# Optimization experiments

Hardware: AMD Instinct MI355X
Metric: run time of the kernel (lower is better)

## Reference

```python
import jax, jax.numpy as jnp
import numpy as np
import math

SR = 96000.0
FRAME = 2048
NB = 16
GAIN_RANGE = (-24.0, 24.0)
Q_RANGE = (0.5, 16.0)
BROADBAND = (-60.0, 0.0)
HPF_R = (20.0, 500.0)
LPF_R = (5000.0, 20000.0)
SHELF_R = (50.0, 16000.0)
PEAK_R = (100.0, 15000.0)


def _dfreq(n, rng):
    lo, hi = math.log(rng[0]), math.log(rng[1])
    return jnp.exp(lo + n * (hi - lo))


def _dgain(n, rng=GAIN_RANGE):
    return rng[0] + n * (rng[1] - rng[0])


def _dq(n):
    lo, hi = math.log(Q_RANGE[0]), math.log(Q_RANGE[1])
    return jnp.exp(lo + n * (hi - lo))


def _coeffs(ftype, fc, gain_db, Q):
    # returns stacked [g, k, a1, a2, a3, m0, m1, m2], each same shape as fc
    g = jnp.clip(jnp.tan(math.pi * fc / SR), 1e-6, 100.0)
    Q = jnp.clip(Q, 0.1, 100.0)
    one = jnp.ones_like(g)
    zero = jnp.zeros_like(g)
    if ftype in ('highpass', 'lowpass'):
        k = 1.0 / Q
        a1 = 1.0 / (1.0 + g * (g + k)); a2 = g * a1; a3 = g * a2
        if ftype == 'highpass':
            m0, m1, m2 = one, -k, -one
        else:
            m0, m1, m2 = zero, zero, one
    elif ftype == 'peak':
        A = jnp.power(10.0, gain_db / 40.0)
        k = jnp.where(gain_db >= 0, 1.0 / (Q * A), A / Q)
        a1 = 1.0 / (1.0 + g * (g + k)); a2 = g * a1; a3 = g * a2
        m0, m1, m2 = one, k * (A * A - 1.0), zero
    elif ftype == 'lowshelf':
        A = jnp.power(10.0, gain_db / 40.0); sA = jnp.sqrt(A); k = 1.0 / Q
        gs = jnp.where(gain_db >= 0, g / sA, g * sA)
        a1 = 1.0 / (1.0 + gs * (gs + k)); a2 = gs * a1; a3 = gs * a2
        m0, m1, m2 = one, k * (A - 1.0), A * A - 1.0
    else:  # highshelf
        A = jnp.power(10.0, gain_db / 40.0); sA = jnp.sqrt(A); k = 1.0 / Q
        gs = jnp.where(gain_db >= 0, g * sA, g / sA)
        a1 = 1.0 / (1.0 + gs * (gs + k)); a2 = gs * a1; a3 = gs * a2
        m0, m1, m2 = A * A, k * (1.0 - A) * A, 1.0 - A * A
    return jnp.stack([g, k, a1, a2, a3, m0, m1, m2], 0)


def _all_coeffs(params, n_frames_audio):
    # params: (B, 50, n_frames_params) -> coeffs (nF, NB, 8, B), in/out gains (nF, B)
    B = params.shape[0]
    nFp = params.shape[2]
    pidx = jnp.minimum(jnp.arange(n_frames_audio), nFp - 1)
    fp = jnp.take(params, pidx, axis=2)                 # (B, 50, nF)
    bq = fp[:, :NB * 3, :].reshape(B, NB, 3, n_frames_audio)
    in_g = jnp.power(10.0, _dgain(fp[:, -2, :], BROADBAND) / 20.0)   # (B, nF)
    out_g = jnp.power(10.0, _dgain(fp[:, -1, :], BROADBAND) / 20.0)  # (B, nF)
    cs = []
    for i in range(NB):
        fn, gn, qn = bq[:, i, 0], bq[:, i, 1], bq[:, i, 2]  # (B, nF)
        Q = _dq(qn)
        if i == 0:
            c = _coeffs('highpass', _dfreq(fn, HPF_R), None, Q)
        elif i == 15:
            c = _coeffs('lowpass', _dfreq(fn, LPF_R), None, Q)
        elif i == 1:
            c = _coeffs('lowshelf', _dfreq(fn, SHELF_R), _dgain(gn), Q)
        elif i == 14:
            c = _coeffs('highshelf', _dfreq(fn, SHELF_R), _dgain(gn), Q)
        else:
            c = _coeffs('peak', _dfreq(fn, PEAK_R), _dgain(gn), Q)
        cs.append(c)  # (8, B, nF)
    coeffs = jnp.transpose(jnp.stack(cs, 0), (3, 0, 1, 2))  # (nF, NB, 8, B)
    return coeffs, in_g.T, out_g.T


def _forward(audio, params):
    B, S = audio.shape
    nF = S // FRAME  # S chosen as exact multiple of FRAME
    coeffs, in_g, out_g = _all_coeffs(params, nF)
    frames = jnp.transpose(audio.reshape(B, nF, FRAME), (1, 2, 0))  # (nF, FRAME, B)

    def frame_step(states, xs):
        fr, c, ig, og = xs  # fr (FRAME,B), c (NB,8,B), ig (B,), og (B,)
        x = fr * ig[None, :]
        new_states = []
        for i in range(NB):
            a1, a2, a3 = c[i, 2], c[i, 3], c[i, 4]
            m0, m1, m2 = c[i, 5], c[i, 6], c[i, 7]

            def samp(st, xn, a1=a1, a2=a2, a3=a3, m0=m0, m1=m1, m2=m2):
                ic1, ic2 = st
                v3 = xn - ic2
                v1 = a1 * ic1 + a2 * v3
                v2 = ic2 + a2 * v1 + a3 * v3
                out = m0 * xn + m1 * v1 + m2 * v2
                return (2.0 * v1 - ic1, 2.0 * v2 - ic2), out

            (ic1, ic2), x = jax.lax.scan(samp, (states[i, 0], states[i, 1]), x)
            new_states.append(jnp.stack([ic1, ic2], 0))
        return jnp.stack(new_states, 0), x * og[None, :]

    init = jnp.zeros((NB, 2, B), audio.dtype)
    _, out = jax.lax.scan(frame_step, init, (frames, coeffs, in_g, out_g))
    return jnp.transpose(out, (2, 0, 1)).reshape(B, S)  # (B, S)


_forward_jit = jax.jit(_forward)


def setup_inputs() -> dict:
    key = jax.random.key(0)
    k1, k2 = jax.random.split(key)
    B, S, nFp = 32, 49152, 24  # 24 frames of 2048 samples
    audio = jax.random.normal(k1, (B, S), dtype=jnp.float32) * 0.1
    params = jax.random.uniform(k2, (B, 50, nFp), dtype=jnp.float32)
    return {'audio': audio, 'params': params}


def reference(audio, params):
    return _forward_jit(audio, params)
```

## Files before the change

### kernel.cpp

```cpp
#include <hip/hip_runtime.h>
#include <math.h>

#define NBATCH 32
#define S      49152
#define NF     24
#define NB     16
#define CHUNK  32
#define NCH    768
#define NWAVE  12

__device__ __forceinline__ float clampf(float x, float lo, float hi) {
    return fminf(fmaxf(x, lo), hi);
}

#define FOREACH_S(OP) \
    OP(s00) OP(s01) OP(s02) OP(s03) OP(s04) OP(s05) OP(s06) OP(s07) \
    OP(s08) OP(s09) OP(s10) OP(s11) OP(s12) OP(s13) OP(s14) OP(s15) \
    OP(s16) OP(s17) OP(s18) OP(s19) OP(s20) OP(s21) OP(s22) OP(s23) \
    OP(s24) OP(s25) OP(s26) OP(s27) OP(s28) OP(s29) OP(s30) OP(s31)

#define DECL_S(x) float x;

#define STEPA(x) { \
    const float n1_ = fmaf(t00, ic1, fmaf(t01, ic2, b0 * (x))); \
    const float n2_ = fmaf(t10, ic1, fmaf(t11, ic2, b1 * (x))); \
    ic1 = n1_; ic2 = n2_; }

#define STEPC(x) { \
    const float y_  = fmaf(c0, ic1, fmaf(c1, ic2, c2 * (x))); \
    const float n1_ = fmaf(t00, ic1, fmaf(t01, ic2, b0 * (x))); \
    const float n2_ = fmaf(t10, ic1, fmaf(t11, ic2, b1 * (x))); \
    (x) = y_; ic1 = n1_; ic2 = n2_; }

__global__ __launch_bounds__(NCH, 3)
void biquad_chain_kernel(const float* __restrict__ audio,
                         const float* __restrict__ params,
                         float* __restrict__ out,
                         unsigned int* __restrict__ ws)
{
    __shared__ float sc[NB][NF][14];
    __shared__ float sgain[2][NF];
    __shared__ float sagg[NWAVE][6];
    __shared__ float sS0[2];

    const int t    = threadIdx.x;
    const int bt   = blockIdx.x >> 1;
    const int half = blockIdx.x & 1;
    const int lane = t & 63;
    const int wave = t >> 6;
    const int g    = half * NCH + t;
    const int frame = half * 12 + wave;

    unsigned int* slotbase = ws + 4 * (bt * NB);

    if (t < NB * NF) {
        const int f  = t / NF;
        const int fr = t % NF;
        const float* P = params + (size_t)bt * 50 * NF;
        const float fn = P[(3 * f + 0) * NF + fr];
        const float gn = P[(3 * f + 1) * NF + fr];
        const float qn = P[(3 * f + 2) * NF + fr];

        float Q = __expf(-0.69314718f + qn * 3.4657359f);
        Q = clampf(Q, 0.1f, 100.0f);

        float lo, hi;
        int type;
        if      (f == 0)  { lo = 20.0f;   hi = 500.0f;   type = 0; }
        else if (f == 15) { lo = 5000.0f; hi = 20000.0f; type = 1; }
        else if (f == 1)  { lo = 50.0f;   hi = 16000.0f; type = 3; }
        else if (f == 14) { lo = 50.0f;   hi = 16000.0f; type = 4; }
        else              { lo = 100.0f;  hi = 15000.0f; type = 2; }

        const float fc = __expf(__logf(lo) + fn * (__logf(hi) - __logf(lo)));
        float g_ = __tanf((float)M_PI * fc / 96000.0f);
        g_ = clampf(g_, 1e-6f, 100.0f);
        const float gdb = -24.0f + 48.0f * gn;

        float a1, a2, a3, m0, m1, m2;
        if (type == 0 || type == 1) {
            const float k = 1.0f / Q;
            a1 = 1.0f / (1.0f + g_ * (g_ + k)); a2 = g_ * a1; a3 = g_ * a2;
            if (type == 0) { m0 = 1.0f; m1 = -k;   m2 = -1.0f; }
            else           { m0 = 0.0f; m1 = 0.0f; m2 = 1.0f;  }
        } else if (type == 2) {
            const float A = __expf(gdb * (2.30258509f / 40.0f));
            const float k = (gdb >= 0.0f) ? 1.0f / (Q * A) : A / Q;
            a1 = 1.0f / (1.0f + g_ * (g_ + k)); a2 = g_ * a1; a3 = g_ * a2;
            m0 = 1.0f; m1 = k * (A * A - 1.0f); m2 = 0.0f;
        } else {
            const float A  = __expf(gdb * (2.30258509f / 40.0f));
            const float sA = sqrtf(A);
            const float k  = 1.0f / Q;
            float gs;
            if (type == 3) gs = (gdb >= 0.0f) ? g_ / sA : g_ * sA;
            else           gs = (gdb >= 0.0f) ? g_ * sA : g_ / sA;
            a1 = 1.0f / (1.0f + gs * (gs + k)); a2 = gs * a1; a3 = gs * a2;
            if (type == 3) { m0 = 1.0f;  m1 = k * (A - 1.0f);      m2 = A * A - 1.0f; }
            else           { m0 = A * A; m1 = k * (1.0f - A) * A;  m2 = 1.0f - A * A; }
        }

        const float q2  = a2 * a2 + a3;
        const float t00 = 2.0f * a1 - 1.0f;
        const float t01 = -2.0f * a2;
        const float t10 = 2.0f * a1 * a2;
        const float t11 = 1.0f - 2.0f * q2;
        const float b0  = 2.0f * a2;
        const float b1  = 2.0f * q2;
        const float c0  = a1 * (m1 + m2 * a2);
        const float c1  = m2 * (1.0f - q2) - m1 * a2;
        const float c2  = m0 + m1 * a2 + m2 * q2;

        float u00 = t00, u01 = t01, u10 = t10, u11 = t11;
        #pragma unroll
        for (int i = 0; i < 5; i++) {
            const float n00 = u00 * u00 + u01 * u10;
            const float n01 = u00 * u01 + u01 * u11;
            const float n10 = u10 * u00 + u11 * u10;
            const float n11 = u10 * u01 + u11 * u11;
            u00 = n00; u01 = n01; u10 = n10; u11 = n11;
        }

        sc[f][fr][0] = t00; sc[f][fr][1] = t01; sc[f][fr][2] = t10; sc[f][fr][3] = t11;
        sc[f][fr][4] = b0;  sc[f][fr][5] = b1;
        sc[f][fr][6] = c0;  sc[f][fr][7] = c1;  sc[f][fr][8] = c2;
        sc[f][fr][9] = u00; sc[f][fr][10] = u01; sc[f][fr][11] = u10; sc[f][fr][12] = u11;
    }
    if (t >= 384 && t < 384 + 2 * NF) {
        const int idx = t - 384;
        const int which = idx / NF;
        const int fr    = idx % NF;
        const float* P = params + (size_t)bt * 50 * NF;
        const float p  = P[(48 + which) * NF + fr];
        const float db = -60.0f + 60.0f * p;
        sgain[which][fr] = __expf(db * (2.30258509f / 20.0f));
    }
    __syncthreads();

    FOREACH_S(DECL_S)
    {
        const float ing = sgain[0][frame];
        const float* base = audio + (size_t)bt * S + (size_t)g * CHUNK;
        float4 q;
        q = *(const float4*)(base +  0); s00 = q.x*ing; s01 = q.y*ing; s02 = q.z*ing; s03 = q.w*ing;
        q = *(const float4*)(base +  4); s04 = q.x*ing; s05 = q.y*ing; s06 = q.z*ing; s07 = q.w*ing;
        q = *(const float4*)(base +  8); s08 = q.x*ing; s09 = q.y*ing; s10 = q.z*ing; s11 = q.w*ing;
        q = *(const float4*)(base + 12); s12 = q.x*ing; s13 = q.y*ing; s14 = q.z*ing; s15 = q.w*ing;
        q = *(const float4*)(base + 16); s16 = q.x*ing; s17 = q.y*ing; s18 = q.z*ing; s19 = q.w*ing;
        q = *(const float4*)(base + 20); s20 = q.x*ing; s21 = q.y*ing; s22 = q.z*ing; s23 = q.w*ing;
        q = *(const float4*)(base + 24); s24 = q.x*ing; s25 = q.y*ing; s26 = q.z*ing; s27 = q.w*ing;
        q = *(const float4*)(base + 28); s28 = q.x*ing; s29 = q.y*ing; s30 = q.z*ing; s31 = q.w*ing;
    }

    #pragma unroll 1
    for (int f = 0; f < NB; f++) {
        const float t00 = sc[f][frame][0];
        const float t01 = sc[f][frame][1];
        const float t10 = sc[f][frame][2];
        const float t11 = sc[f][frame][3];
        const float b0  = sc[f][frame][4];
        const float b1  = sc[f][frame][5];
        const float c0  = sc[f][frame][6];
        const float c1  = sc[f][frame][7];
        const float c2  = sc[f][frame][8];

        float ic1 = 0.0f, ic2 = 0.0f;
        FOREACH_S(STEPA)

        float A00 = sc[f][frame][9];
        float A01 = sc[f][frame][10];
        float A10 = sc[f][frame][11];
        float A11 = sc[f][frame][12];
        float Ac0 = ic1, Ac1 = ic2;
        #pragma unroll
        for (int d = 1; d < 64; d <<= 1) {
            const float l00 = __shfl_up(A00, d);
            const float l01 = __shfl_up(A01, d);
            const float l10 = __shfl_up(A10, d);
            const float l11 = __shfl_up(A11, d);
            const float lc0 = __shfl_up(Ac0, d);
            const float lc1 = __shfl_up(Ac1, d);
            if (lane >= d) {
                const float n00 = A00 * l00 + A01 * l10;
                const float n01 = A00 * l01 + A01 * l11;
                const float n10 = A10 * l00 + A11 * l10;
                const float n11 = A10 * l01 + A11 * l11;
                const float nc0 = A00 * lc0 + A01 * lc1 + Ac0;
                const float nc1 = A10 * lc0 + A11 * lc1 + Ac1;
                A00 = n00; A01 = n01; A10 = n10; A11 = n11;
                Ac0 = nc0; Ac1 = nc1;
            }
        }

        __syncthreads();
        if (lane == 63) {
            sagg[wave][0] = A00; sagg[wave][1] = A01;
            sagg[wave][2] = A10; sagg[wave][3] = A11;
            sagg[wave][4] = Ac0; sagg[wave][5] = Ac1;
        }
        __syncthreads();

        float W00 = 1.0f, W01 = 0.0f, W10 = 0.0f, W11 = 1.0f, Wc0 = 0.0f, Wc1 = 0.0f;
        for (int k2 = 0; k2 < wave; k2++) {
            const float g00 = sagg[k2][0], g01 = sagg[k2][1];
            const float g10 = sagg[k2][2], g11 = sagg[k2][3];
            const float gc0 = sagg[k2][4], gc1 = sagg[k2][5];
            const float n00 = g00 * W00 + g01 * W10;
            const float n01 = g00 * W01 + g01 * W11;
            const float n10 = g10 * W00 + g11 * W10;
            const float n11 = g10 * W01 + g11 * W11;
            const float nc0 = g00 * Wc0 + g01 * Wc1 + gc0;
            const float nc1 = g10 * Wc0 + g11 * Wc1 + gc1;
            W00 = n00; W01 = n01; W10 = n10; W11 = n11;
            Wc0 = nc0; Wc1 = nc1;
        }

        const unsigned int tag = (unsigned int)(f + 1);
        unsigned int* slot = slotbase + 4 * f;

        if (half == 0) {
            if (t == NCH - 1) {
                const float e0 = A00 * Wc0 + A01 * Wc1 + Ac0;
                const float e1 = A10 * Wc0 + A11 * Wc1 + Ac1;
                float* datap = (float*)(slot + 1);
                __hip_atomic_store(&datap[0], e0, __ATOMIC_RELAXED, __HIP_MEMORY_SCOPE_AGENT);
                __hip_atomic_store(&datap[1], e1, __ATOMIC_RELAXED, __HIP_MEMORY_SCOPE_AGENT);
                __hip_atomic_store(slot, tag, __ATOMIC_RELEASE, __HIP_MEMORY_SCOPE_AGENT);
            }
        }

        float S0x = 0.0f, S0y = 0.0f;
        if (half == 1) {
            if (t == 0) {
                while (__hip_atomic_load(slot, __ATOMIC_ACQUIRE, __HIP_MEMORY_SCOPE_AGENT) != tag) {
                    __builtin_amdgcn_s_sleep(2);
                }
                float* datap = (float*)(slot + 1);
                sS0[0] = __hip_atomic_load(&datap[0], __ATOMIC_RELAXED, __HIP_MEMORY_SCOPE_AGENT);
                sS0[1] = __hip_atomic_load(&datap[1], __ATOMIC_RELAXED, __HIP_MEMORY_SCOPE_AGENT);
            }
            __syncthreads();
            S0x = sS0[0];
            S0y = sS0[1];
        }

        float P00 = __shfl_up(A00, 1);
        float P01 = __shfl_up(A01, 1);
        float P10 = __shfl_up(A10, 1);
        float P11 = __shfl_up(A11, 1);
        float Pc0 = __shfl_up(Ac0, 1);
        float Pc1 = __shfl_up(Ac1, 1);
        if (lane == 0) { P00 = 1.0f; P01 = 0.0f; P10 = 0.0f; P11 = 1.0f; Pc0 = 0.0f; Pc1 = 0.0f; }
        const float E00 = P00 * W00 + P01 * W10;
        const float E01 = P00 * W01 + P01 * W11;
        const float E10 = P10 * W00 + P11 * W10;
        const float E11 = P10 * W01 + P11 * W11;
        const float Ec0 = P00 * Wc0 + P01 * Wc1 + Pc0;
        const float Ec1 = P10 * Wc0 + P11 * Wc1 + Pc1;

        ic1 = E00 * S0x + E01 * S0y + Ec0;
        ic2 = E10 * S0x + E11 * S0y + Ec1;
        FOREACH_S(STEPC)
    }

    {
        const float og = sgain[1][frame];
        float* base = out + (size_t)bt * S + (size_t)g * CHUNK;
        float4 q;
        q.x = s00*og; q.y = s01*og; q.z = s02*og; q.w = s03*og; *(float4*)(base +  0) = q;
        q.x = s04*og; q.y = s05*og; q.z = s06*og; q.w = s07*og; *(float4*)(base +  4) = q;
        q.x = s08*og; q.y = s09*og; q.z = s10*og; q.w = s11*og; *(float4*)(base +  8) = q;
        q.x = s12*og; q.y = s13*og; q.z = s14*og; q.w = s15*og; *(float4*)(base + 12) = q;
        q.x = s16*og; q.y = s17*og; q.z = s18*og; q.w = s19*og; *(float4*)(base + 16) = q;
        q.x = s20*og; q.y = s21*og; q.z = s22*og; q.w = s23*og; *(float4*)(base + 20) = q;
        q.x = s24*og; q.y = s25*og; q.z = s26*og; q.w = s27*og; *(float4*)(base + 24) = q;
        q.x = s28*og; q.y = s29*og; q.z = s30*og; q.w = s31*og; *(float4*)(base + 28) = q;
    }
}

extern "C" void kernel_launch(void* const* d_in, const int* in_sizes, int n_in,
                              void* d_out, int out_size, void* d_ws, size_t ws_size,
                              hipStream_t stream)
{
    const float* audio  = (const float*)d_in[0];
    const float* params = (const float*)d_in[1];
    float* out = (float*)d_out;
    unsigned int* ws = (unsigned int*)d_ws;
    biquad_chain_kernel<<<2 * NBATCH, NCH, 0, stream>>>(audio, params, out, ws);
}
```

Measured before the change: 137.8 us.

## Split each batch row across four blocks with a cross-block scan chain

New measurement: 137.2 us. Within noise of the previous version (-0.4%).

```diff
diff --git a/kernel.cpp b/kernel.cpp
--- a/kernel.cpp
+++ b/kernel.cpp
@@ -5,7 +5,8 @@
 #define S      49152
 #define NF     24
 #define NB     16
-#define CHUNK  32
+#define NBLK   4
+#define CHUNK  16
 #define NCH    768
 #define NWAVE  12
 
@@ -15,9 +16,7 @@
 
 #define FOREACH_S(OP) \
     OP(s00) OP(s01) OP(s02) OP(s03) OP(s04) OP(s05) OP(s06) OP(s07) \
-    OP(s08) OP(s09) OP(s10) OP(s11) OP(s12) OP(s13) OP(s14) OP(s15) \
-    OP(s16) OP(s17) OP(s18) OP(s19) OP(s20) OP(s21) OP(s22) OP(s23) \
-    OP(s24) OP(s25) OP(s26) OP(s27) OP(s28) OP(s29) OP(s30) OP(s31)
+    OP(s08) OP(s09) OP(s10) OP(s11) OP(s12) OP(s13) OP(s14) OP(s15)
 
 #define DECL_S(x) float x;
 
@@ -40,18 +39,15 @@
 {
     __shared__ float sc[NB][NF][14];
     __shared__ float sgain[2][NF];
-    __shared__ float sagg[NWAVE][6];
-    __shared__ float sS0[2];
-
-    const int t    = threadIdx.x;
-    const int bt   = blockIdx.x >> 1;
-    const int half = blockIdx.x & 1;
-    const int lane = t & 63;
-    const int wave = t >> 6;
-    const int g    = half * NCH + t;
-    const int frame = half * 12 + wave;
-
-    unsigned int* slotbase = ws + 4 * (bt * NB);
+    __shared__ float sagg[2][NWAVE][6];
+    __shared__ float sS0[2][2];
+
+    const int t       = threadIdx.x;
+    const int bt      = blockIdx.x >> 2;
+    const int quarter = blockIdx.x & 3;
+    const int lane    = t & 63;
+    const int wave    = t >> 6;
+    const int frame   = quarter * 6 + (wave >> 1);
 
     if (t < NB * NF) {
         const int f  = t / NF;
@@ -113,7 +109,7 @@
 
         float u00 = t00, u01 = t01, u10 = t10, u11 = t11;
         #pragma unroll
-        for (int i = 0; i < 5; i++) {
+        for (int i = 0; i < 4; i++) {
             const float n00 = u00 * u00 + u01 * u10;
             const float n01 = u00 * u01 + u01 * u11;
             const float n10 = u10 * u00 + u11 * u10;
@@ -140,20 +136,18 @@
     FOREACH_S(DECL_S)
     {
         const float ing = sgain[0][frame];
-        const float* base = audio + (size_t)bt * S + (size_t)g * CHUNK;
+        const float* base = audio + (size_t)bt * S
+                          + (size_t)(quarter * NCH + t) * CHUNK;
         float4 q;
         q = *(const float4*)(base +  0); s00 = q.x*ing; s01 = q.y*ing; s02 = q.z*ing; s03 = q.w*ing;
         q = *(const float4*)(base +  4); s04 = q.x*ing; s05 = q.y*ing; s06 = q.z*ing; s07 = q.w*ing;
         q = *(const float4*)(base +  8); s08 = q.x*ing; s09 = q.y*ing; s10 = q.z*ing; s11 = q.w*ing;
         q = *(const float4*)(base + 12); s12 = q.x*ing; s13 = q.y*ing; s14 = q.z*ing; s15 = q.w*ing;
-        q = *(const float4*)(base + 16); s16 = q.x*ing; s17 = q.y*ing; s18 = q.z*ing; s19 = q.w*ing;
-        q = *(const float4*)(base + 20); s20 = q.x*ing; s21 = q.y*ing; s22 = q.z*ing; s23 = q.w*ing;
-        q = *(const float4*)(base + 24); s24 = q.x*ing; s25 = q.y*ing; s26 = q.z*ing; s27 = q.w*ing;
-        q = *(const float4*)(base + 28); s28 = q.x*ing; s29 = q.y*ing; s30 = q.z*ing; s31 = q.w*ing;
     }
 
     #pragma unroll 1
     for (int f = 0; f < NB; f++) {
+        const int buf = f & 1;
         const float t00 = sc[f][frame][0];
         const float t01 = sc[f][frame][1];
         const float t10 = sc[f][frame][2];
@@ -192,57 +186,92 @@
             }
         }
 
+        if (lane == 63) {
+            sagg[buf][wave][0] = A00; sagg[buf][wave][1] = A01;
+            sagg[buf][wave][2] = A10; sagg[buf][wave][3] = A11;
+            sagg[buf][wave][4] = Ac0; sagg[buf][wave][5] = Ac1;
+        }
         __syncthreads();
-        if (lane == 63) {
-            sagg[wave][0] = A00; sagg[wave][1] = A01;
-            sagg[wave][2] = A10; sagg[wave][3] = A11;
-            sagg[wave][4] = Ac0; sagg[wave][5] = Ac1;
-        }
-        __syncthreads();
-
-        float W00 = 1.0f, W01 = 0.0f, W10 = 0.0f, W11 = 1.0f, Wc0 = 0.0f, Wc1 = 0.0f;
-        for (int k2 = 0; k2 < wave; k2++) {
-            const float g00 = sagg[k2][0], g01 = sagg[k2][1];
-            const float g10 = sagg[k2][2], g11 = sagg[k2][3];
-            const float gc0 = sagg[k2][4], gc1 = sagg[k2][5];
-            const float n00 = g00 * W00 + g01 * W10;
-            const float n01 = g00 * W01 + g01 * W11;
-            const float n10 = g10 * W00 + g11 * W10;
-            const float n11 = g10 * W01 + g11 * W11;
-            const float nc0 = g00 * Wc0 + g01 * Wc1 + gc0;
-            const float nc1 = g10 * Wc0 + g11 * Wc1 + gc1;
-            W00 = n00; W01 = n01; W10 = n10; W11 = n11;
-            Wc0 = nc0; Wc1 = nc1;
+
+        float G00 = 1.0f, G01 = 0.0f, G10 = 0.0f, G11 = 1.0f, Gc0 = 0.0f, Gc1 = 0.0f;
+        if (lane < NWAVE) {
+            G00 = sagg[buf][lane][0]; G01 = sagg[buf][lane][1];
+            G10 = sagg[buf][lane][2]; G11 = sagg[buf][lane][3];
+            Gc0 = sagg[buf][lane][4]; Gc1 = sagg[buf][lane][5];
+        }
+        #pragma unroll
+        for (int d = 1; d < 16; d <<= 1) {
+            const float l00 = __shfl_up(G00, d);
+            const float l01 = __shfl_up(G01, d);
+            const float l10 = __shfl_up(G10, d);
+            const float l11 = __shfl_up(G11, d);
+            const float lc0 = __shfl_up(Gc0, d);
+            const float lc1 = __shfl_up(Gc1, d);
+            if (lane >= d && lane < NWAVE) {
+                const float n00 = G00 * l00 + G01 * l10;
+                const float n01 = G00 * l01 + G01 * l11;
+                const float n10 = G10 * l00 + G11 * l10;
+                const float n11 = G10 * l01 + G11 * l11;
+                const float nc0 = G00 * lc0 + G01 * lc1 + Gc0;
+                const float nc1 = G10 * lc0 + G11 * lc1 + Gc1;
+                G00 = n00; G01 = n01; G10 = n10; G11 = n11;
+                Gc0 = nc0; Gc1 = nc1;
+            }
         }
 
         const unsigned int tag = (unsigned int)(f + 1);
-        unsigned int* slot = slotbase + 4 * f;
-
-        if (half == 0) {
-            if (t == NCH - 1) {
-                const float e0 = A00 * Wc0 + A01 * Wc1 + Ac0;
-                const float e1 = A10 * Wc0 + A11 * Wc1 + Ac1;
-                float* datap = (float*)(slot + 1);
-                __hip_atomic_store(&datap[0], e0, __ATOMIC_RELAXED, __HIP_MEMORY_SCOPE_AGENT);
-                __hip_atomic_store(&datap[1], e1, __ATOMIC_RELAXED, __HIP_MEMORY_SCOPE_AGENT);
-                __hip_atomic_store(slot, tag, __ATOMIC_RELEASE, __HIP_MEMORY_SCOPE_AGENT);
-            }
+        unsigned int* stagebase = ws + ((bt * NB + f) * NBLK) * 8;
+
+        if (quarter < NBLK - 1 && wave == 0 && lane == NWAVE - 1) {
+            unsigned int* slot = stagebase + quarter * 8;
+            float* dp = (float*)(slot + 1);
+            __hip_atomic_store(&dp[0], G00, __ATOMIC_RELAXED, __HIP_MEMORY_SCOPE_AGENT);
+            __hip_atomic_store(&dp[1], G01, __ATOMIC_RELAXED, __HIP_MEMORY_SCOPE_AGENT);
+            __hip_atomic_store(&dp[2], G10, __ATOMIC_RELAXED, __HIP_MEMORY_SCOPE_AGENT);
+            __hip_atomic_store(&dp[3], G11, __ATOMIC_RELAXED, __HIP_MEMORY_SCOPE_AGENT);
+            __hip_atomic_store(&dp[4], Gc0, __ATOMIC_RELAXED, __HIP_MEMORY_SCOPE_AGENT);
+            __hip_atomic_store(&dp[5], Gc1, __ATOMIC_RELAXED, __HIP_MEMORY_SCOPE_AGENT);
+            __hip_atomic_store(slot, tag, __ATOMIC_RELEASE, __HIP_MEMORY_SCOPE_AGENT);
         }
 
         float S0x = 0.0f, S0y = 0.0f;
-        if (half == 1) {
+        if (quarter > 0) {
             if (t == 0) {
-                while (__hip_atomic_load(slot, __ATOMIC_ACQUIRE, __HIP_MEMORY_SCOPE_AGENT) != tag) {
-                    __builtin_amdgcn_s_sleep(2);
+                float sx = 0.0f, sy = 0.0f;
+                for (int k2 = 0; k2 < quarter; k2++) {
+                    unsigned int* slot = stagebase + k2 * 8;
+                    while (__hip_atomic_load(slot, __ATOMIC_ACQUIRE, __HIP_MEMORY_SCOPE_AGENT) != tag) {
+                        __builtin_amdgcn_s_sleep(2);
+                    }
+                    float* dp = (float*)(slot + 1);
+                    const float m00 = __hip_atomic_load(&dp[0], __ATOMIC_RELAXED, __HIP_MEMORY_SCOPE_AGENT);
+                    const float m01 = __hip_atomic_load(&dp[1], __ATOMIC_RELAXED, __HIP_MEMORY_SCOPE_AGENT);
+                    const float m10 = __hip_atomic_load(&dp[2], __ATOMIC_RELAXED, __HIP_MEMORY_SCOPE_AGENT);
+                    const float m11 = __hip_atomic_load(&dp[3], __ATOMIC_RELAXED, __HIP_MEMORY_SCOPE_AGENT);
+                    const float cc0 = __hip_atomic_load(&dp[4], __ATOMIC_RELAXED, __HIP_MEMORY_SCOPE_AGENT);
+                    const float cc1 = __hip_atomic_load(&dp[5], __ATOMIC_RELAXED, __HIP_MEMORY_SCOPE_AGENT);
+                    const float nx = m00 * sx + m01 * sy + cc0;
+                    const float ny = m10 * sx + m11 * sy + cc1;
+                    sx = nx; sy = ny;
                 }
-                float* datap = (float*)(slot + 1);
-                sS0[0] = __hip_atomic_load(&datap[0], __ATOMIC_RELAXED, __HIP_MEMORY_SCOPE_AGENT);
-                sS0[1] = __hip_atomic_load(&datap[1], __ATOMIC_RELAXED, __HIP_MEMORY_SCOPE_AGENT);
+                sS0[buf][0] = sx; sS0[buf][1] = sy;
             }
             __syncthreads();
-            S0x = sS0[0];
-            S0y = sS0[1];
-        }
+            S0x = sS0[buf][0];
+            S0y = sS0[buf][1];
+        }
+
+        const int wsrc = (wave > 0) ? (wave - 1) : 0;
+        float Wm00 = __shfl(G00, wsrc);
+        float Wm01 = __shfl(G01, wsrc);
+        float Wm10 = __shfl(G10, wsrc);
+        float Wm11 = __shfl(G11, wsrc);
+        float Wc0  = __shfl(Gc0, wsrc);
+        float Wc1  = __shfl(Gc1, wsrc);
+        if (wave == 0) { Wm00 = 1.0f; Wm01 = 0.0f; Wm10 = 0.0f; Wm11 = 1.0f; Wc0 = 0.0f; Wc1 = 0.0f; }
+
+        const float vx = Wm00 * S0x + Wm01 * S0y + Wc0;
+        const float vy = Wm10 * S0x + Wm11 * S0y + Wc1;
 
         float P00 = __shfl_up(A00, 1);
         float P01 = __shfl_up(A01, 1);
@@ -251,30 +280,20 @@
         float Pc0 = __shfl_up(Ac0, 1);
         float Pc1 = __shfl_up(Ac1, 1);
         if (lane == 0) { P00 = 1.0f; P01 = 0.0f; P10 = 0.0f; P11 = 1.0f; Pc0 = 0.0f; Pc1 = 0.0f; }
-        const float E00 = P00 * W00 + P01 * W10;
-        const float E01 = P00 * W01 + P01 * W11;
-        const float E10 = P10 * W00 + P11 * W10;
-        const float E11 = P10 * W01 + P11 * W11;
-        const float Ec0 = P00 * Wc0 + P01 * Wc1 + Pc0;
-        const float Ec1 = P10 * Wc0 + P11 * Wc1 + Pc1;
-
-        ic1 = E00 * S0x + E01 * S0y + Ec0;
-        ic2 = E10 * S0x + E11 * S0y + Ec1;
+        ic1 = P00 * vx + P01 * vy + Pc0;
+        ic2 = P10 * vx + P11 * vy + Pc1;
+
         FOREACH_S(STEPC)
     }
 
     {
         const float og = sgain[1][frame];
-        float* base = out + (size_t)bt * S + (size_t)g * CHUNK;
+        float* base = out + (size_t)bt * S + (size_t)(quarter * NCH + t) * CHUNK;
         float4 q;
         q.x = s00*og; q.y = s01*og; q.z = s02*og; q.w = s03*og; *(float4*)(base +  0) = q;
         q.x = s04*og; q.y = s05*og; q.z = s06*og; q.w = s07*og; *(float4*)(base +  4) = q;
         q.x = s08*og; q.y = s09*og; q.z = s10*og; q.w = s11*og; *(float4*)(base +  8) = q;
         q.x = s12*og; q.y = s13*og; q.z = s14*og; q.w = s15*og; *(float4*)(base + 12) = q;
-        q.x = s16*og; q.y = s17*og; q.z = s18*og; q.w = s19*og; *(float4*)(base + 16) = q;
-        q.x = s20*og; q.y = s21*og; q.z = s22*og; q.w = s23*og; *(float4*)(base + 20) = q;
-        q.x = s24*og; q.y = s25*og; q.z = s26*og; q.w = s27*og; *(float4*)(base + 24) = q;
-        q.x = s28*og; q.y = s29*og; q.z = s30*og; q.w = s31*og; *(float4*)(base + 28) = q;
     }
 }
 
@@ -286,5 +305,5 @@
     const float* params = (const float*)d_in[1];
     float* out = (float*)d_out;
     unsigned int* ws = (unsigned int*)d_ws;
-    biquad_chain_kernel<<<2 * NBATCH, NCH, 0, stream>>>(audio, params, out, ws);
+    biquad_chain_kernel<<<NBLK * NBATCH, NCH, 0, stream>>>(audio, params, out, ws);
 }
```
